# Kernel tuning notes

Measured on AMD Instinct MI355X. Metric: run time of the kernel, lower is better.

Reference implementation:

```python
import jax, jax.numpy as jnp
import numpy as np

B, S, C = 2, 4096, 1280        # batch, spatial tokens, hidden_size
CA = 2048                      # cross_attention_dim
HEADS = 20
HD = C // HEADS                # head_dim = 64
N_TXT, N_OBJ, N_OTH, N_IP = 77, 4, 4, 16
SCALE_OBJ = SCALE_OTH = SCALE_IP = 1.0
RESCALE = 1.0


def _heads(x):
    # [B, L, C] -> [B, H, L, hd]
    b, l, _ = x.shape
    return x.reshape(b, l, HEADS, HD).transpose(0, 2, 1, 3)


def _merge(x):
    # [B, H, L, hd] -> [B, L, C]
    b, h, l, d = x.shape
    return x.transpose(0, 2, 1, 3).reshape(b, l, h * d)


def _sdpa(q, k, v):
    scale = 1.0 / np.sqrt(HD).astype(np.float32)
    s = jnp.einsum('bhqd,bhkd->bhqk', q, k) * scale
    p = jax.nn.softmax(s, axis=-1)
    return jnp.einsum('bhqk,bhkd->bhqd', p, v)


def setup_inputs() -> dict:
    key = jax.random.key(0)
    ks = jax.random.split(key, 16)
    g = lambda k, shp, fan: jax.random.normal(k, shp, jnp.float32) / np.sqrt(fan).astype(np.float32)
    return {
        'hidden_states': jax.random.normal(ks[0], (B, S, C), jnp.float32),
        'encoder_hidden_states': jax.random.normal(ks[1], (B, N_TXT + N_OBJ + N_OTH + N_IP, CA), jnp.float32),
        # weights stored [in, out] (x @ W)
        'to_q_w': g(ks[2], (C, C), C),
        'to_k_w': g(ks[3], (CA, C), CA),
        'to_v_w': g(ks[4], (CA, C), CA),
        'to_k_object_w': g(ks[5], (CA, C), CA),
        'to_v_object_w': g(ks[6], (CA, C), CA),
        'to_k_others_w': g(ks[7], (CA, C), CA),
        'to_v_others_w': g(ks[8], (CA, C), CA),
        'to_k_ip_w': g(ks[9], (CA, C), CA),
        'to_v_ip_w': g(ks[10], (CA, C), CA),
        'to_out_w': g(ks[11], (C, C), C),
        'to_out_b': jnp.zeros((C,), jnp.float32),
    }


def reference(hidden_states, encoder_hidden_states, to_q_w, to_k_w, to_v_w,
              to_k_object_w, to_v_object_w, to_k_others_w, to_v_others_w,
              to_k_ip_w, to_v_ip_w, to_out_w, to_out_b):
    residual = hidden_states
    # split encoder states: text | object | others | ip
    end = N_TXT
    ehs_txt = encoder_hidden_states[:, :end]
    ehs_obj = encoder_hidden_states[:, end:end + N_OBJ]
    ehs_oth = encoder_hidden_states[:, end + N_OBJ:end + N_OBJ + N_OTH]
    ehs_ip = encoder_hidden_states[:, end + N_OBJ + N_OTH:]

    q = _heads(hidden_states @ to_q_w)                       # [B,H,S,hd]

    # main text cross-attention
    h_txt = _sdpa(q, _heads(ehs_txt @ to_k_w), _heads(ehs_txt @ to_v_w))
    # object / others / ip branches (tiny KV)
    h_obj = _sdpa(q, _heads(ehs_obj @ to_k_object_w), _heads(ehs_obj @ to_v_object_w))
    h_oth = _sdpa(q, _heads(ehs_oth @ to_k_others_w), _heads(ehs_oth @ to_v_others_w))
    h_ip = _sdpa(q, _heads(ehs_ip @ to_k_ip_w), _heads(ehs_ip @ to_v_ip_w))

    out = _merge(h_txt) + SCALE_OBJ * _merge(h_obj) + SCALE_OTH * _merge(h_oth) + SCALE_IP * _merge(h_ip)
    out = out @ to_out_w + to_out_b                          # to_out[0]; to_out[1] is dropout=identity
    out = (out + residual) / RESCALE                         # residual_connection=True
    return out
```

## Files before the change

kernel.cpp:

```cpp
#include <hip/hip_runtime.h>
#include <stdint.h>

typedef unsigned short u16;
typedef __attribute__((ext_vector_type(8))) short short8;
typedef __attribute__((ext_vector_type(4))) short short4b;
typedef __attribute__((ext_vector_type(4))) float f32x4;

#define MFMA16 __builtin_amdgcn_mfma_f32_16x16x32_bf16

__device__ __forceinline__ u16 f2b(float f) {
  union { float f; uint32_t i; } x; x.f = f;
  uint32_t r = x.i + 0x7FFFu + ((x.i >> 16) & 1u);
  return (u16)(r >> 16);
}
__device__ __forceinline__ float b2f(u16 u) {
  union { uint32_t i; float f; } x; x.i = ((uint32_t)u) << 16; return x.f;
}

__device__ __forceinline__ void gload16(const u16* g, u16* l) {
  __builtin_amdgcn_global_load_lds(
      (const __attribute__((address_space(1))) void*)g,
      (__attribute__((address_space(3))) void*)l, 16, 0, 0);
}

__global__ __launch_bounds__(256) void cvt_k(const float* __restrict__ src,
                                             u16* __restrict__ dst, int n) {
  const int i = (blockIdx.x * 256 + threadIdx.x) * 4;
  if (i < n) {
    const float4 v = *(const float4*)(src + i);
    dst[i + 0] = f2b(v.x); dst[i + 1] = f2b(v.y);
    dst[i + 2] = f2b(v.z); dst[i + 3] = f2b(v.w);
  }
}

struct TransArgs { const float* src[2]; u16* dst[2]; };

__global__ __launch_bounds__(512) void transpose_k(TransArgs a) {
  const int m = blockIdx.z;
  const int r0 = blockIdx.y * 64;
  const int c0 = blockIdx.x * 64;
  const float* src = a.src[m];
  u16* dst = a.dst[m];
  __shared__ u16 t[64][65];
  const int tx = threadIdx.x, ty = threadIdx.y;
#pragma unroll
  for (int i = 0; i < 64; i += 8)
    t[ty + i][tx] = f2b(src[(size_t)(r0 + ty + i) * 1280 + c0 + tx]);
  __syncthreads();
#pragma unroll
  for (int i = 0; i < 64; i += 8)
    dst[(size_t)(c0 + ty + i) * 1280 + r0 + tx] = t[tx][ty + i];
}

template <bool F32OUT>
__global__ __launch_bounds__(256) void gemm_bt(
    const u16* __restrict__ A, const u16* __restrict__ BT,
    u16* __restrict__ C16, float* __restrict__ C32,
    int M, int N, int K,
    const float* __restrict__ bias, const float* __restrict__ resid) {
  __shared__ __align__(16) u16 As[8192];
  __shared__ __align__(16) u16 Bs[8192];
  const int tid = threadIdx.x;
  const int w = tid >> 6, lane = tid & 63;
  const int l15 = lane & 15, quad = lane >> 4;
  const int m0 = blockIdx.x * 128, n0 = blockIdx.y * 128;
  const int wm = w >> 1, wn = w & 1;

  const int rowa = tid >> 3;
  const int cgx = (tid & 7) ^ (rowa & 7);
  const u16* pa = A  + (size_t)(m0 + rowa) * K + cgx * 8;
  const u16* pb = BT + (size_t)(n0 + rowa) * K + cgx * 8;
  u16* la = As + tid * 8;
  u16* lb = Bs + tid * 8;

  f32x4 acc[4][4];
#pragma unroll
  for (int i = 0; i < 4; i++)
#pragma unroll
    for (int j = 0; j < 4; j++) acc[i][j] = (f32x4){0.f, 0.f, 0.f, 0.f};

  for (int kt = 0; kt < K; kt += 64) {
#pragma unroll
    for (int s = 0; s < 4; s++) {
      const size_t go = (size_t)(s * 32) * K + kt;
      gload16(pa + go, la + s * 2048);
      gload16(pb + go, lb + s * 2048);
    }
    __syncthreads();

#pragma unroll
    for (int ks = 0; ks < 2; ks++) {
      short8 af[4], bfr[4];
#pragma unroll
      for (int i = 0; i < 4; i++) {
        const int arow = wm * 64 + i * 16 + l15;
        const int brow = wn * 64 + i * 16 + l15;
        const int ch = ((ks * 4 + quad) ^ (l15 & 7)) * 8;
        af[i]  = *(const short8*)(As + arow * 64 + ch);
        bfr[i] = *(const short8*)(Bs + brow * 64 + ch);
      }
#pragma unroll
      for (int i = 0; i < 4; i++)
#pragma unroll
        for (int j = 0; j < 4; j++)
          acc[i][j] = MFMA16(af[i], bfr[j], acc[i][j], 0, 0, 0);
    }
    __syncthreads();
  }

#pragma unroll
  for (int i = 0; i < 4; i++) {
    const int row0 = m0 + wm * 64 + i * 16 + quad * 4;
#pragma unroll
    for (int j = 0; j < 4; j++) {
      const int col = n0 + wn * 64 + j * 16 + l15;
      const float bv2 = F32OUT ? bias[col] : 0.f;
#pragma unroll
      for (int r = 0; r < 4; r++) {
        const size_t idx = (size_t)(row0 + r) * N + col;
        if (F32OUT) {
          C32[idx] = acc[i][j][r] + bv2 + resid[idx];
        } else {
          C16[idx] = f2b(acc[i][j][r]);
        }
      }
    }
  }
}

struct KVArgs {
  const float* ehs;
  const float* w[8];
  u16* Kws;
  u16* VTws;
};

__global__ __launch_bounds__(256) void kv_proj(KVArgs a) {
  const int bx = blockIdx.x;
  const int b = bx >> 4;
  const int r = bx & 15;
  int mat, mt;
  if (r < 5)       { mat = 0; mt = r; }
  else if (r < 10) { mat = 1; mt = r - 5; }
  else             { mat = 2 + (r - 10); mt = 0; }
  const int seg = mat >> 1;
  const int soff4[4] = {0, 77, 81, 85};
  const int slen4[4] = {77, 4, 4, 16};
  const int soff = soff4[seg], slen = slen4[seg];
  const int n0 = blockIdx.y * 64;
  const int tid = threadIdx.x;
  const int w = tid >> 6;
  const int lane = tid & 63, l15 = lane & 15, quad = lane >> 4;
  int tl = mt * 16 + l15; if (tl >= slen) tl = slen - 1;
  const float* Arow = a.ehs + ((size_t)b * 101 + soff + tl) * 2048;
  const float* W = a.w[mat];
  f32x4 acc = (f32x4){0.f, 0.f, 0.f, 0.f};
  for (int k = 0; k < 2048; k += 32) {
    const float4 a0 = *(const float4*)(Arow + k + quad * 8);
    const float4 a1 = *(const float4*)(Arow + k + quad * 8 + 4);
    short8 af;
    af[0] = (short)f2b(a0.x); af[1] = (short)f2b(a0.y);
    af[2] = (short)f2b(a0.z); af[3] = (short)f2b(a0.w);
    af[4] = (short)f2b(a1.x); af[5] = (short)f2b(a1.y);
    af[6] = (short)f2b(a1.z); af[7] = (short)f2b(a1.w);
    const float* wcol = W + (size_t)(k + quad * 8) * 1280 + n0 + w * 16 + l15;
    short8 bf_;
#pragma unroll
    for (int j = 0; j < 8; j++) bf_[j] = (short)f2b(wcol[(size_t)j * 1280]);
    acc = MFMA16(af, bf_, acc, 0, 0, 0);
  }
  const bool isK = !(mat & 1);
#pragma unroll
  for (int rr = 0; rr < 4; rr++) {
    const int tloc = mt * 16 + quad * 4 + rr;
    if (tloc >= slen) continue;
    const int key = soff + tloc;
    const int col = n0 + w * 16 + l15;
    const u16 v = f2b(acc[rr]);
    if (isK) {
      a.Kws[((size_t)b * 101 + key) * 1280 + col] = v;
    } else {
      const int hh = col >> 6, dd = col & 63;
      a.VTws[((size_t)(b * 20 + hh) * 64 + dd) * 128 + key] = v;
    }
  }
}

__global__ __launch_bounds__(256) void attn_k(
    const u16* __restrict__ Q, const u16* __restrict__ Kws,
    const u16* __restrict__ VT, u16* __restrict__ O) {
  const int s0 = blockIdx.x * 64;
  const int h  = blockIdx.y;
  const int b  = blockIdx.z;
  const int tid = threadIdx.x;
  const int w = tid >> 6, lane = tid & 63, l15 = lane & 15, quad = lane >> 4;

  __shared__ __align__(16) u16 KP[8192];
  __shared__ __align__(16) u16 Vt[8192];

  for (int e = tid; e < 7168; e += 256) {
    const int key = e >> 6, d = e & 63;
    u16 v = 0;
    if (key < 101) v = Kws[((size_t)b * 101 + key) * 1280 + h * 64 + d];
    const int off = ((key >> 4) * 2 + (d >> 5)) * 512 + ((d >> 3) & 3) * 128 + (key & 15) * 8 + (d & 7);
    KP[off] = v;
  }
  for (int e = tid; e < 8192; e += 256) {
    const int d = e >> 7, key = e & 127;
    u16 v = 0;
    if (key < 101) v = VT[((size_t)(b * 20 + h) * 64 + d) * 128 + key];
    const int off = ((d >> 4) * 4 + (key >> 5)) * 512 + ((key >> 3) & 3) * 128 + (d & 15) * 8 + (key & 7);
    Vt[off] = v;
  }
  const u16* qrow = Q + ((size_t)b * 4096 + s0 + w * 16 + l15) * 1280 + h * 64;
  const short8 qf0 = *(const short8*)(qrow + quad * 8);
  const short8 qf1 = *(const short8*)(qrow + 32 + quad * 8);
  __syncthreads();

  f32x4 sc[7];
#pragma unroll
  for (int t = 0; t < 7; t++) {
    f32x4 a = (f32x4){0.f, 0.f, 0.f, 0.f};
    const short8 k0 = *(const short8*)(KP + (t * 2 + 0) * 512 + quad * 128 + l15 * 8);
    const short8 k1 = *(const short8*)(KP + (t * 2 + 1) * 512 + quad * 128 + l15 * 8);
    a = MFMA16(k0, qf0, a, 0, 0, 0);
    a = MFMA16(k1, qf1, a, 0, 0, 0);
    sc[t] = a;
  }

  float sv[7][4];
#pragma unroll
  for (int t = 0; t < 7; t++)
#pragma unroll
    for (int r = 0; r < 4; r++) sv[t][r] = sc[t][r] * 0.125f;

  const int kb = quad * 4;
  float mx0 = -1e30f, mx1 = -1e30f, mx2 = -1e30f, mx3 = -1e30f;
#pragma unroll
  for (int t = 0; t < 7; t++)
#pragma unroll
    for (int r = 0; r < 4; r++) {
      const int key = t * 16 + kb + r;
      const float v = sv[t][r];
      if (key < 77)       mx0 = fmaxf(mx0, v);
      else if (key < 81)  mx1 = fmaxf(mx1, v);
      else if (key < 85)  mx2 = fmaxf(mx2, v);
      else if (key < 101) mx3 = fmaxf(mx3, v);
    }
  mx0 = fmaxf(mx0, __shfl_xor(mx0, 16, 64)); mx0 = fmaxf(mx0, __shfl_xor(mx0, 32, 64));
  mx1 = fmaxf(mx1, __shfl_xor(mx1, 16, 64)); mx1 = fmaxf(mx1, __shfl_xor(mx1, 32, 64));
  mx2 = fmaxf(mx2, __shfl_xor(mx2, 16, 64)); mx2 = fmaxf(mx2, __shfl_xor(mx2, 32, 64));
  mx3 = fmaxf(mx3, __shfl_xor(mx3, 16, 64)); mx3 = fmaxf(mx3, __shfl_xor(mx3, 32, 64));

  float sm0 = 0.f, sm1 = 0.f, sm2 = 0.f, sm3 = 0.f;
#pragma unroll
  for (int t = 0; t < 7; t++)
#pragma unroll
    for (int r = 0; r < 4; r++) {
      const int key = t * 16 + kb + r;
      float e = 0.f;
      if (key < 77)       { e = __expf(sv[t][r] - mx0); sm0 += e; }
      else if (key < 81)  { e = __expf(sv[t][r] - mx1); sm1 += e; }
      else if (key < 85)  { e = __expf(sv[t][r] - mx2); sm2 += e; }
      else if (key < 101) { e = __expf(sv[t][r] - mx3); sm3 += e; }
      sv[t][r] = e;
    }
  sm0 += __shfl_xor(sm0, 16, 64); sm0 += __shfl_xor(sm0, 32, 64);
  sm1 += __shfl_xor(sm1, 16, 64); sm1 += __shfl_xor(sm1, 32, 64);
  sm2 += __shfl_xor(sm2, 16, 64); sm2 += __shfl_xor(sm2, 32, 64);
  sm3 += __shfl_xor(sm3, 16, 64); sm3 += __shfl_xor(sm3, 32, 64);
  const float inv0 = 1.f / sm0, inv1 = 1.f / sm1, inv2 = 1.f / sm2, inv3 = 1.f / sm3;
#pragma unroll
  for (int t = 0; t < 7; t++)
#pragma unroll
    for (int r = 0; r < 4; r++) {
      const int key = t * 16 + kb + r;
      const float f = key < 77 ? inv0 : key < 81 ? inv1 : key < 85 ? inv2 : inv3;
      sv[t][r] *= f;
    }

  __syncthreads();

#pragma unroll
  for (int t = 0; t < 7; t++) {
    const int key0 = t * 16 + kb;
    const int off = (w * 4 + (key0 >> 5)) * 512 + ((key0 >> 3) & 3) * 128 + l15 * 8 + (key0 & 7);
    short4b pv;
    pv[0] = (short)f2b(sv[t][0]); pv[1] = (short)f2b(sv[t][1]);
    pv[2] = (short)f2b(sv[t][2]); pv[3] = (short)f2b(sv[t][3]);
    *(short4b*)(KP + off) = pv;
  }
  if (quad < 2)
    *(short8*)(KP + (w * 4 + 3) * 512 + (quad + 2) * 128 + l15 * 8) =
        (short8){0, 0, 0, 0, 0, 0, 0, 0};

  f32x4 oacc[4];
#pragma unroll
  for (int dsm = 0; dsm < 4; dsm++) oacc[dsm] = (f32x4){0.f, 0.f, 0.f, 0.f};
#pragma unroll
  for (int ks = 0; ks < 4; ks++) {
    const short8 pf = *(const short8*)(KP + (w * 4 + ks) * 512 + quad * 128 + l15 * 8);
#pragma unroll
    for (int dsm = 0; dsm < 4; dsm++) {
      const short8 vf = *(const short8*)(Vt + (dsm * 4 + ks) * 512 + quad * 128 + l15 * 8);
      oacc[dsm] = MFMA16(pf, vf, oacc[dsm], 0, 0, 0);
    }
  }
  u16* orow = O + ((size_t)b * 4096 + s0 + w * 16) * 1280 + h * 64;
#pragma unroll
  for (int dsm = 0; dsm < 4; dsm++)
#pragma unroll
    for (int r = 0; r < 4; r++)
      orow[(size_t)(quad * 4 + r) * 1280 + dsm * 16 + l15] = f2b(oacc[dsm][r]);
}

extern "C" void kernel_launch(void* const* d_in, const int* in_sizes, int n_in,
                              void* d_out, int out_size, void* d_ws, size_t ws_size,
                              hipStream_t stream) {
  const float* HS  = (const float*)d_in[0];
  const float* EHS = (const float*)d_in[1];
  const float* Wq  = (const float*)d_in[2];
  const float* Wo  = (const float*)d_in[11];
  const float* Bo  = (const float*)d_in[12];

  u16* ws = (u16*)d_ws;
  u16* HSb  = ws;                      ws += (size_t)8192 * 1280;
  u16* AO   = HSb;
  u16* WqT  = ws;                      ws += (size_t)1280 * 1280;
  u16* WoT  = ws;                      ws += (size_t)1280 * 1280;
  u16* Kws  = ws;                      ws += (size_t)2 * 101 * 1280;
  u16* VTw  = ws;                      ws += (size_t)2 * 20 * 64 * 128;
  u16* Qb   = (u16*)d_out;
  (void)ws_size; (void)in_sizes; (void)n_in; (void)out_size;

  cvt_k<<<dim3(8192 * 1280 / 4 / 256), 256, 0, stream>>>(HS, HSb, 8192 * 1280);

  TransArgs ta;
  ta.src[0] = Wq; ta.dst[0] = WqT;
  ta.src[1] = Wo; ta.dst[1] = WoT;
  transpose_k<<<dim3(20, 20, 2), dim3(64, 8), 0, stream>>>(ta);

  gemm_bt<false><<<dim3(64, 10), 256, 0, stream>>>(HSb, WqT, Qb, nullptr,
                                                   8192, 1280, 1280, nullptr, nullptr);

  KVArgs ka;
  ka.ehs = EHS;
  for (int i = 0; i < 8; i++) ka.w[i] = (const float*)d_in[3 + i];
  ka.Kws = Kws; ka.VTws = VTw;
  kv_proj<<<dim3(32, 20), 256, 0, stream>>>(ka);

  attn_k<<<dim3(64, 20, 2), 256, 0, stream>>>(Qb, Kws, VTw, AO);

  gemm_bt<true><<<dim3(64, 10), 256, 0, stream>>>(AO, WoT, nullptr, (float*)d_out,
                                                  8192, 1280, 1280, Bo, HS);
}
```

Measured before the change: 411.4 us.

## Stage KV-projection weight and activation tiles through swizzled LDS with register prefetch

The kv_proj kernel previously had each lane read eight strided scalar weight values per MFMA step directly from global memory, which gives poorly coalesced loads. It now loads 64x64 weight tiles and 16x64 activation tiles with coalesced float4 reads, converts them to bf16, and transposes them into XOR-swizzled shared memory. MFMA operands are then read as short8 vectors. The next tile is prefetched into registers while the current one is computed, at the cost of two barriers per iteration and extra LDS stores.

```diff
diff --git a/kernel.cpp b/kernel.cpp
--- a/kernel.cpp
+++ b/kernel.cpp
@@ -151,24 +151,69 @@
   const int tid = threadIdx.x;
   const int w = tid >> 6;
   const int lane = tid & 63, l15 = lane & 15, quad = lane >> 4;
-  int tl = mt * 16 + l15; if (tl >= slen) tl = slen - 1;
-  const float* Arow = a.ehs + ((size_t)b * 101 + soff + tl) * 2048;
   const float* W = a.w[mat];
+
+  __shared__ __align__(16) u16 Wt[4096];
+  __shared__ __align__(16) u16 At[1024];
+
+  const int ar = tid >> 4, af4 = tid & 15;
+  int tok = mt * 16 + ar; if (tok >= slen) tok = slen - 1;
+  const float* Arow = a.ehs + ((size_t)b * 101 + soff + tok) * 2048;
+
+  float4 wreg[4]; float4 areg;
+#pragma unroll
+  for (int rep = 0; rep < 4; rep++) {
+    const int idx = rep * 256 + tid;
+    const int kr = idx >> 4, f4 = idx & 15;
+    wreg[rep] = *(const float4*)(W + (size_t)kr * 1280 + n0 + f4 * 4);
+  }
+  areg = *(const float4*)(Arow + af4 * 4);
+
   f32x4 acc = (f32x4){0.f, 0.f, 0.f, 0.f};
-  for (int k = 0; k < 2048; k += 32) {
-    const float4 a0 = *(const float4*)(Arow + k + quad * 8);
-    const float4 a1 = *(const float4*)(Arow + k + quad * 8 + 4);
-    short8 af;
-    af[0] = (short)f2b(a0.x); af[1] = (short)f2b(a0.y);
-    af[2] = (short)f2b(a0.z); af[3] = (short)f2b(a0.w);
-    af[4] = (short)f2b(a1.x); af[5] = (short)f2b(a1.y);
-    af[6] = (short)f2b(a1.z); af[7] = (short)f2b(a1.w);
-    const float* wcol = W + (size_t)(k + quad * 8) * 1280 + n0 + w * 16 + l15;
-    short8 bf_;
-#pragma unroll
-    for (int j = 0; j < 8; j++) bf_[j] = (short)f2b(wcol[(size_t)j * 1280]);
-    acc = MFMA16(af, bf_, acc, 0, 0, 0);
-  }
+  const int colw = w * 16 + l15;
+  const int colp = (colw + (colw >> 3)) & 7;
+
+  for (int t = 0; t < 32; ++t) {
+#pragma unroll
+    for (int rep = 0; rep < 4; rep++) {
+      const int idx = rep * 256 + tid;
+      const int kr = idx >> 4, f4 = idx & 15;
+      const float wsv[4] = {wreg[rep].x, wreg[rep].y, wreg[rep].z, wreg[rep].w};
+#pragma unroll
+      for (int i = 0; i < 4; i++) {
+        const int col = f4 * 4 + i;
+        const int oct = (kr >> 3) ^ ((col + (col >> 3)) & 7);
+        Wt[col * 64 + oct * 8 + (kr & 7)] = f2b(wsv[i]);
+      }
+    }
+    {
+      short4b av4;
+      av4[0] = (short)f2b(areg.x); av4[1] = (short)f2b(areg.y);
+      av4[2] = (short)f2b(areg.z); av4[3] = (short)f2b(areg.w);
+      *(short4b*)(At + ar * 64 + (((af4 >> 1) ^ (ar & 7)) * 8) + (af4 & 1) * 4) = av4;
+    }
+    __syncthreads();
+
+    if (t + 1 < 32) {
+      const int k0 = (t + 1) * 64;
+#pragma unroll
+      for (int rep = 0; rep < 4; rep++) {
+        const int idx = rep * 256 + tid;
+        const int kr = idx >> 4, f4 = idx & 15;
+        wreg[rep] = *(const float4*)(W + (size_t)(k0 + kr) * 1280 + n0 + f4 * 4);
+      }
+      areg = *(const float4*)(Arow + k0 + af4 * 4);
+    }
+
+#pragma unroll
+    for (int ks = 0; ks < 2; ks++) {
+      const short8 af = *(const short8*)(At + l15 * 64 + (((ks * 4 + quad) ^ (l15 & 7)) * 8));
+      const short8 bf = *(const short8*)(Wt + colw * 64 + (((ks * 4 + quad) ^ colp) * 8));
+      acc = MFMA16(af, bf, acc, 0, 0, 0);
+    }
+    __syncthreads();
+  }
+
   const bool isK = !(mat & 1);
 #pragma unroll
   for (int rr = 0; rr < 4; rr++) {
```

Result: faster. 369.4 us (-10.2%).
